# Optimization experiments

Measured on AMD Instinct MI355X. Metric: run time of the kernel, lower is better.

Reference implementation:

```python
import jax, jax.numpy as jnp
import numpy as np

B, D, E, H = 2048, 1024, 32, 1024  # tokens, hidden, total experts (m*N), ffn_dim_small


def setup_inputs() -> dict:
    key = jax.random.key(0)
    ks = jax.random.split(key, 5)
    scale_in = 1.0 / np.sqrt(D)
    scale_h = 1.0 / np.sqrt(H)
    return {
        "x": jax.random.normal(ks[0], (B, D), dtype=jnp.float32),
        "Wg": jax.random.normal(ks[1], (D, E), dtype=jnp.float32) * scale_in,
        "W1": jax.random.normal(ks[2], (E, D, H), dtype=jnp.float32) * scale_in,
        "b1": jnp.zeros((E, H), dtype=jnp.float32),
        "W2": jax.random.normal(ks[3], (E, H, D), dtype=jnp.float32) * scale_h,
        "b2": jnp.zeros((E, D), dtype=jnp.float32),
        "topk": 8,  # m * K
    }


def reference(x, Wg, W1, b1, W2, b2, topk):
    # gating: softmax then keep only top-k probs (others zeroed), no renorm
    logits = x @ Wg                                   # [B, E]
    probs = jax.nn.softmax(logits, axis=-1)           # [B, E]
    _, idx = jax.lax.top_k(probs, topk)               # [B, topk]
    mask = jnp.zeros_like(probs).at[jnp.arange(x.shape[0])[:, None], idx].set(1.0)
    gate = probs * mask                               # [B, E]

    # dense all-expert FFN (faithful to original which runs every expert)
    h = jax.nn.relu(jnp.einsum('bd,edh->beh', x, W1) + b1)   # [B, E, H]
    y = jnp.einsum('beh,ehd->bed', h, W2) + b2               # [B, E, D]

    moe_out = jnp.einsum('be,bed->bd', gate, y)              # weighted sum over experts
    return x + moe_out
```

## Files before the change

### kernel.cpp

```cpp
#include <hip/hip_runtime.h>
#include <hip/hip_bf16.h>

#define B_TOK 2048
#define DDIM 1024
#define NEXP 32
#define HDIM 1024
#define TOPK 8
#define PITCH 1088

typedef __bf16 bf16_t;
typedef __bf16 bf16x8 __attribute__((ext_vector_type(8)));
typedef float f32x4 __attribute__((ext_vector_type(4)));

__global__ __launch_bounds__(256) void k_prep(const float* __restrict__ x,
                                              bf16_t* __restrict__ xb,
                                              float* __restrict__ out) {
  int i = (blockIdx.x * 256 + threadIdx.x) * 8;
  float4 v0 = *(const float4*)&x[i];
  float4 v1 = *(const float4*)&x[i + 4];
  bf16x8 v;
  v[0] = (bf16_t)v0.x; v[1] = (bf16_t)v0.y; v[2] = (bf16_t)v0.z; v[3] = (bf16_t)v0.w;
  v[4] = (bf16_t)v1.x; v[5] = (bf16_t)v1.y; v[6] = (bf16_t)v1.z; v[7] = (bf16_t)v1.w;
  int row = i >> 10, col = i & 1023;
  *(bf16x8*)&xb[(size_t)row * PITCH + col] = v;
  *(float4*)&out[i] = v0;
  *(float4*)&out[i + 4] = v1;
}

__global__ __launch_bounds__(256) void k_gating(const float* __restrict__ x,
                                                const float* __restrict__ Wg,
                                                int* __restrict__ sel_e,
                                                float* __restrict__ sel_w) {
  int token = blockIdx.x * 4 + (threadIdx.x >> 6);
  int lane = threadIdx.x & 63;
  int e = lane & 31;
  int half = lane >> 5;
  const float* xr = x + (size_t)token * DDIM + half * (DDIM / 2);
  const float* wg = Wg + (size_t)half * (DDIM / 2) * NEXP + e;
  float acc = 0.f;
#pragma unroll 8
  for (int k = 0; k < DDIM / 2; ++k) acc = fmaf(xr[k], wg[k * NEXP], acc);
  acc += __shfl_xor(acc, 32);
  float m = acc;
  for (int off = 16; off; off >>= 1) m = fmaxf(m, __shfl_xor(m, off));
  float p = __expf(acc - m);
  float s = p;
  for (int off = 16; off; off >>= 1) s += __shfl_xor(s, off);
  p /= s;
  float pv = p;
  int my_se = 0;
  float my_sw = 0.f;
  for (int it = 0; it < TOPK; ++it) {
    float mx = pv;
    for (int off = 16; off; off >>= 1) mx = fmaxf(mx, __shfl_xor(mx, off));
    unsigned long long bal = __ballot(pv == mx);
    int sl = __ffsll(bal) - 1;
    int se = sl & 31;
    if (lane == it) { my_se = se; my_sw = mx; }
    if (e == se) pv = -1.f;
  }
  if (lane < TOPK) {
    sel_e[token * TOPK + lane] = my_se;
    sel_w[token * TOPK + lane] = my_sw;
  }
}

__global__ __launch_bounds__(256) void k_build_lists(const int* __restrict__ sel_e,
                                                     const float* __restrict__ sel_w,
                                                     int* __restrict__ list,
                                                     float* __restrict__ wlist,
                                                     int* __restrict__ count) {
  int e = blockIdx.x;
  int t = threadIdx.x;
  int lane = t & 63, wv = t >> 6;
  __shared__ int wsum[4];
  __shared__ int base;
  if (t == 0) base = 0;
  __syncthreads();
  for (int c = 0; c < B_TOK; c += 256) {
    int b = c + t;
    int flag = 0, slot = 0;
    float w = 0.f;
#pragma unroll
    for (int j = 0; j < TOPK; ++j) {
      if (sel_e[b * TOPK + j] == e) { flag = 1; slot = j; w = sel_w[b * TOPK + j]; }
    }
    unsigned long long bal = __ballot(flag);
    int pre = __popcll(bal & ((1ull << lane) - 1ull));
    int tot = __popcll(bal);
    if (lane == 0) wsum[wv] = tot;
    __syncthreads();
    int off = base;
    for (int i = 0; i < wv; ++i) off += wsum[i];
    if (flag) {
      int pos = off + pre;
      list[e * B_TOK + pos] = (b << 3) | slot;
      wlist[e * B_TOK + pos] = w;
    }
    __syncthreads();
    if (t == 0) base += wsum[0] + wsum[1] + wsum[2] + wsum[3];
    __syncthreads();
  }
  if (t == 0) count[e] = base;
}

__global__ __launch_bounds__(64) void k_build_queue(const int* __restrict__ count,
                                                    int* __restrict__ queue,
                                                    int* __restrict__ qn) {
  int e = threadIdx.x;
  int nmt = 0;
  if (e < NEXP) nmt = (count[e] + 127) >> 7;
  int pref = 0, tot = 0;
  for (int i = 0; i < NEXP; ++i) {
    int v = __shfl(nmt, i);
    if (i < e) pref += v;
    tot += v;
  }
  if (e < NEXP) {
    int base = pref * 8;
    for (int y = 0; y < 8; ++y)
      for (int mt = 0; mt < nmt; ++mt)
        queue[base + y * nmt + mt] = (e << 8) | (mt << 3) | y;
  }
  if (threadIdx.x == 0) qn[0] = tot * 8;
}

__device__ __forceinline__ void async_load16(const bf16_t* g, bf16_t* l) {
  __builtin_amdgcn_global_load_lds((const __attribute__((address_space(1))) void*)g,
                                   (__attribute__((address_space(3))) void*)l, 16, 0, 0);
}

template <int PHASE>
__global__ __launch_bounds__(256, 3) void k_gemm(const bf16_t* __restrict__ Abase,
                                                 const float* __restrict__ Wraw,
                                                 const int* __restrict__ list,
                                                 const float* __restrict__ wlist,
                                                 const int* __restrict__ count,
                                                 const int* __restrict__ queue,
                                                 const int* __restrict__ qn,
                                                 const float* __restrict__ bias,
                                                 bf16_t* __restrict__ hbuf,
                                                 float* __restrict__ out) {
  __shared__ bf16_t As[128][64];
  __shared__ bf16_t Bs[128][64];

  const int phys = blockIdx.x;
  const int nwg = qn[0];
  if (phys >= nwg) return;
  const int q8 = nwg >> 3, r8 = nwg & 7;
  const int xcd = phys & 7, loc = phys >> 3;
  const int wk = (xcd < r8 ? xcd * (q8 + 1) : r8 * (q8 + 1) + (xcd - r8) * q8) + loc;

  const int ent = queue[wk];
  const int e = ent >> 8;
  const int mt = (ent >> 3) & 31;
  const int y = ent & 7;

  const int cnt = count[e];
  const int m0 = mt * 128;
  const int n0 = y * 128;

  const int t = threadIdx.x;
  const int lane = t & 63;
  const int w = t >> 6;
  const int wm = (w >> 1) << 6;
  const int wc = (w & 1) << 6;
  const int lr = lane & 15;
  const int hi = lane >> 4;
  const int l7 = lane & 7;
  const int srs = ((lane & 7) ^ (lane >> 3)) << 3;

  const int* lrow = list + e * B_TOK;

  const bf16_t* aptr[4];
#pragma unroll
  for (int i = 0; i < 4; ++i) {
    int mi = m0 + w * 32 + i * 8 + (lane >> 3);
    if (mi > cnt - 1) mi = cnt - 1;
    int li = lrow[mi];
    int tok = li >> 3, slot = li & 7;
    size_t arow = (PHASE == 1) ? (size_t)tok * PITCH : ((size_t)tok * 8 + slot) * PITCH;
    aptr[i] = Abase + arow + srs;
  }

  const int cB = t & 31;
  const int aB = t >> 5;
  const float* bcol = Wraw + (size_t)e * DDIM * HDIM + n0 + cB * 4;

  f32x4 acc[4][4] = {};

#pragma unroll 1
  for (int kt = 0; kt < 16; ++kt) {
#pragma unroll
    for (int i = 0; i < 4; ++i)
      async_load16(aptr[i] + kt * 64, &As[w * 32 + i * 8][0]);
    {
      const float* p = bcol + (size_t)(kt * 64 + aB * 8) * 1024;
      float4 v[8];
#pragma unroll
      for (int kk = 0; kk < 8; ++kk)
        v[kk] = *(const float4*)(p + (size_t)kk * 1024);
#pragma unroll
      for (int jn = 0; jn < 4; ++jn) {
        const int n = cB * 4 + jn;
        bf16x8 pk;
#pragma unroll
        for (int kk = 0; kk < 8; ++kk) pk[kk] = (bf16_t)(((const float*)&v[kk])[jn]);
        *(bf16x8*)&Bs[n][(aB ^ (n & 7)) << 3] = pk;
      }
    }
    __syncthreads();
    bf16x8 af[4][2], bfr[4][2];
#pragma unroll
    for (int ks = 0; ks < 2; ++ks) {
      const int ca = (((ks << 2) | hi) ^ l7) << 3;
#pragma unroll
      for (int m = 0; m < 4; ++m)
        af[m][ks] = *(const bf16x8*)&As[wm + m * 16 + lr][ca];
#pragma unroll
      for (int n = 0; n < 4; ++n)
        bfr[n][ks] = *(const bf16x8*)&Bs[wc + n * 16 + lr][ca];
    }
#pragma unroll
    for (int m = 0; m < 4; ++m)
#pragma unroll
      for (int n = 0; n < 4; ++n)
#pragma unroll
        for (int ks = 0; ks < 2; ++ks)
          acc[m][n] = __builtin_amdgcn_mfma_f32_16x16x32_bf16(af[m][ks], bfr[n][ks], acc[m][n], 0, 0, 0);
    __syncthreads();
  }

  float biasv[4];
#pragma unroll
  for (int n = 0; n < 4; ++n) biasv[n] = bias[e * 1024 + n0 + wc + n * 16 + lr];

#pragma unroll
  for (int m = 0; m < 4; ++m) {
#pragma unroll
    for (int j = 0; j < 4; ++j) {
      int gm = m0 + wm + m * 16 + hi * 4 + j;
      if (gm < cnt) {
        int li2 = lrow[gm];
        int tok2 = li2 >> 3, slot2 = li2 & 7;
        if (PHASE == 1) {
          bf16_t* hr = hbuf + ((size_t)tok2 * 8 + slot2) * PITCH + n0 + wc + lr;
#pragma unroll
          for (int n = 0; n < 4; ++n) {
            float v = acc[m][n][j] + biasv[n];
            hr[n * 16] = (bf16_t)(v > 0.f ? v : 0.f);
          }
        } else {
          float gw = wlist[e * B_TOK + gm];
          float* orow = out + (size_t)tok2 * DDIM + n0 + wc + lr;
#pragma unroll
          for (int n = 0; n < 4; ++n) {
            float v = (acc[m][n][j] + biasv[n]) * gw;
            unsafeAtomicAdd(&orow[n * 16], v);
          }
        }
      }
    }
  }
}

extern "C" void kernel_launch(void* const* d_in, const int* in_sizes, int n_in,
                              void* d_out, int out_size, void* d_ws, size_t ws_size,
                              hipStream_t stream) {
  const float* x = (const float*)d_in[0];
  const float* Wg = (const float*)d_in[1];
  const float* W1 = (const float*)d_in[2];
  const float* b1 = (const float*)d_in[3];
  const float* W2 = (const float*)d_in[4];
  const float* b2 = (const float*)d_in[5];
  float* out = (float*)d_out;

  char* ws = (char*)d_ws;
  bf16_t* xb = (bf16_t*)ws;   ws += (size_t)B_TOK * PITCH * 2;
  bf16_t* hbuf = (bf16_t*)ws; ws += (size_t)B_TOK * TOPK * PITCH * 2;
  int* sel_e = (int*)ws;      ws += (size_t)B_TOK * TOPK * 4;
  float* sel_w = (float*)ws;  ws += (size_t)B_TOK * TOPK * 4;
  int* list = (int*)ws;       ws += (size_t)NEXP * B_TOK * 4;
  float* wlist = (float*)ws;  ws += (size_t)NEXP * B_TOK * 4;
  int* count = (int*)ws;      ws += 64 * 4;
  int* queue = (int*)ws;      ws += 2048 * 4;
  int* qn = (int*)ws;         ws += 64 * 4;

  k_prep<<<1024, 256, 0, stream>>>(x, xb, out);
  k_gating<<<512, 256, 0, stream>>>(x, Wg, sel_e, sel_w);
  k_build_lists<<<32, 256, 0, stream>>>(sel_e, sel_w, list, wlist, count);
  k_build_queue<<<1, 64, 0, stream>>>(count, queue, qn);
  k_gemm<1><<<1536, 256, 0, stream>>>(xb, W1, list, wlist, count, queue, qn, b1, hbuf, out);
  k_gemm<2><<<1536, 256, 0, stream>>>(hbuf, W2, list, wlist, count, queue, qn, b2, hbuf, out);
}
```

Measured before the change: 268.2 us.

## Prefetch next B tile into registers during MFMA and split B loads into float2 halves

Software-pipelines the fp32 weight loads: the next k-tile of W is loaded into registers before the current tile's MFMAs run, so global latency overlaps compute. The loop is unrolled by two with ping-pong register sets. Each thread now loads two float2 columns 64 apart instead of one float4, which changes the B column mapping and the bank pattern of LDS writes. This adds 32 more VGPRs, which may hurt occupancy under launch_bounds(256,3).

```diff
diff --git a/kernel.cpp b/kernel.cpp
--- a/kernel.cpp
+++ b/kernel.cpp
@@ -130,6 +130,50 @@
                                    (__attribute__((address_space(3))) void*)l, 16, 0, 0);
 }
 
+#define LOADB(LO, HI, KT)                                                     \
+  {                                                                           \
+    const float* p_ = bcol + (size_t)((KT)*64 + aB * 8) * 1024;               \
+    _Pragma("unroll") for (int kk = 0; kk < 8; ++kk) {                        \
+      LO[kk] = *(const float2*)(p_ + (size_t)kk * 1024);                      \
+      HI[kk] = *(const float2*)(p_ + (size_t)kk * 1024 + 64);                 \
+    }                                                                         \
+  }
+
+#define CVTWRITE(LO, HI)                                                      \
+  {                                                                           \
+    _Pragma("unroll") for (int jn = 0; jn < 4; ++jn) {                        \
+      const int n = (jn < 2) ? (2 * qB + jn) : (64 + 2 * qB + (jn - 2));      \
+      bf16x8 pk;                                                              \
+      _Pragma("unroll") for (int kk = 0; kk < 8; ++kk)                        \
+          pk[kk] = (bf16_t)((jn == 0) ? LO[kk].x : (jn == 1) ? LO[kk].y       \
+                            : (jn == 2) ? HI[kk].x : HI[kk].y);               \
+      *(bf16x8*)&Bs[n][(aB ^ (n & 7)) << 3] = pk;                             \
+    }                                                                         \
+  }
+
+#define ISSUE_A(KT)                                                           \
+  {                                                                           \
+    _Pragma("unroll") for (int i = 0; i < 4; ++i)                             \
+        async_load16(aptr[i] + (KT)*64, &As[w * 32 + i * 8][0]);              \
+  }
+
+#define MFMA_PHASE()                                                          \
+  {                                                                           \
+    bf16x8 af[4][2], bfr[4][2];                                               \
+    _Pragma("unroll") for (int ks = 0; ks < 2; ++ks) {                        \
+      const int ca = (((ks << 2) | hi) ^ l7) << 3;                            \
+      _Pragma("unroll") for (int m = 0; m < 4; ++m)                           \
+          af[m][ks] = *(const bf16x8*)&As[wm + m * 16 + lr][ca];              \
+      _Pragma("unroll") for (int n = 0; n < 4; ++n)                           \
+          bfr[n][ks] = *(const bf16x8*)&Bs[wc + n * 16 + lr][ca];             \
+    }                                                                         \
+    _Pragma("unroll") for (int m = 0; m < 4; ++m)                             \
+        _Pragma("unroll") for (int n = 0; n < 4; ++n)                         \
+            _Pragma("unroll") for (int ks = 0; ks < 2; ++ks)                  \
+                acc[m][n] = __builtin_amdgcn_mfma_f32_16x16x32_bf16(          \
+                    af[m][ks], bfr[n][ks], acc[m][n], 0, 0, 0);               \
+  }
+
 template <int PHASE>
 __global__ __launch_bounds__(256, 3) void k_gemm(const bf16_t* __restrict__ Abase,
                                                  const float* __restrict__ Wraw,
@@ -183,51 +227,30 @@
     aptr[i] = Abase + arow + srs;
   }
 
-  const int cB = t & 31;
+  const int qB = t & 31;
   const int aB = t >> 5;
-  const float* bcol = Wraw + (size_t)e * DDIM * HDIM + n0 + cB * 4;
+  const float* bcol = Wraw + (size_t)e * DDIM * HDIM + n0 + 2 * qB;
 
   f32x4 acc[4][4] = {};
+  float2 valo[8], vahi[8], vblo[8], vbhi[8];
+
+  LOADB(valo, vahi, 0)
 
 #pragma unroll 1
-  for (int kt = 0; kt < 16; ++kt) {
-#pragma unroll
-    for (int i = 0; i < 4; ++i)
-      async_load16(aptr[i] + kt * 64, &As[w * 32 + i * 8][0]);
-    {
-      const float* p = bcol + (size_t)(kt * 64 + aB * 8) * 1024;
-      float4 v[8];
-#pragma unroll
-      for (int kk = 0; kk < 8; ++kk)
-        v[kk] = *(const float4*)(p + (size_t)kk * 1024);
-#pragma unroll
-      for (int jn = 0; jn < 4; ++jn) {
-        const int n = cB * 4 + jn;
-        bf16x8 pk;
-#pragma unroll
-        for (int kk = 0; kk < 8; ++kk) pk[kk] = (bf16_t)(((const float*)&v[kk])[jn]);
-        *(bf16x8*)&Bs[n][(aB ^ (n & 7)) << 3] = pk;
-      }
-    }
-    __syncthreads();
-    bf16x8 af[4][2], bfr[4][2];
-#pragma unroll
-    for (int ks = 0; ks < 2; ++ks) {
-      const int ca = (((ks << 2) | hi) ^ l7) << 3;
-#pragma unroll
-      for (int m = 0; m < 4; ++m)
-        af[m][ks] = *(const bf16x8*)&As[wm + m * 16 + lr][ca];
-#pragma unroll
-      for (int n = 0; n < 4; ++n)
-        bfr[n][ks] = *(const bf16x8*)&Bs[wc + n * 16 + lr][ca];
-    }
-#pragma unroll
-    for (int m = 0; m < 4; ++m)
-#pragma unroll
-      for (int n = 0; n < 4; ++n)
-#pragma unroll
-        for (int ks = 0; ks < 2; ++ks)
-          acc[m][n] = __builtin_amdgcn_mfma_f32_16x16x32_bf16(af[m][ks], bfr[n][ks], acc[m][n], 0, 0, 0);
+  for (int kt2 = 0; kt2 < 8; ++kt2) {
+    const int ktA = kt2 * 2;
+    const int ktB = ktA + 1;
+    ISSUE_A(ktA)
+    CVTWRITE(valo, vahi)
+    __syncthreads();
+    LOADB(vblo, vbhi, ktB)
+    MFMA_PHASE()
+    __syncthreads();
+    ISSUE_A(ktB)
+    CVTWRITE(vblo, vbhi)
+    __syncthreads();
+    if (ktB < 15) LOADB(valo, vahi, ktB + 1)
+    MFMA_PHASE()
     __syncthreads();
   }
 
```

After: 255.8 us (median of 2 runs). 1.05x faster.
